# Performance work log

Hardware: AMD Instinct MI355X
Metric: run time of the kernel (lower is better)

The kernel has to match this reference:

```python
import jax, jax.numpy as jnp
import numpy as np

C = 32
SHIFTS = (1, 2, 4)
KSIZE = 4  # trans_layer: kernel KSIZE+1, stride KSIZE, pad KSIZE//2
EPS_NORM = 1e-12
EPS_BN = 1e-5


def _make_diff_kernels(c):
    # 8 fixed 3x3 difference kernels, tiled per channel for depthwise conv.
    d1 = np.array([[[-1, 0, 0], [0, 1, 0], [0, 0, 0]],
                   [[0, -1, 0], [0, 1, 0], [0, 0, 0]],
                   [[0, 0, -1], [0, 1, 0], [0, 0, 0]],
                   [[0, 0, 0], [0, 1, -1], [0, 0, 0]]], dtype=np.float32)
    d1 = d1.reshape(4, 1, 3, 3)
    d2 = d1[:, :, ::-1, ::-1].copy()
    delta = np.concatenate([d1, d2], axis=0)          # [8,1,3,3]
    return jnp.asarray(np.tile(delta, (c, 1, 1, 1)))  # [8C,1,3,3]


DIFF_KERNELS = _make_diff_kernels(C)


def conv2d(x, w, stride=1, pad=0, dilation=1, groups=1):
    return jax.lax.conv_general_dilated(
        x, w, (stride, stride), [(pad, pad), (pad, pad)],
        rhs_dilation=(dilation, dilation),
        dimension_numbers=('NCHW', 'OIHW', 'NCHW'),
        feature_group_count=groups)


def l2norm(x, axis=-1):
    n = jnp.sqrt(jnp.sum(x * x, axis=axis, keepdims=True))
    return x / jnp.maximum(n, EPS_NORM)


def setup_inputs() -> dict:
    key = jax.random.key(0)
    ks = jax.random.split(key, 8)
    S = len(SHIFTS)
    return {
        'cen': jax.random.normal(ks[0], (2, C, 256, 256), jnp.float32),
        'trans_W': jax.random.normal(ks[1], (C, C, 5, 5), jnp.float32) * 0.05,
        'trans_b': jax.random.normal(ks[2], (C,), jnp.float32) * 0.05,
        'query_W': jax.random.normal(ks[3], (C, C, 1, 1), jnp.float32) * 0.05,
        'value_W': jax.random.normal(ks[4], (S, C, C, 1, 1), jnp.float32) * 0.05,
        'key_W': jax.random.normal(ks[5], (S, C, C, 1, 1), jnp.float32) * 0.05,
        'out_W': jax.random.normal(ks[6], (C, C, 1, 1), jnp.float32) * 0.05,
        'bn_gamma': jnp.ones((C,), jnp.float32),
        'bn_beta': jnp.zeros((C,), jnp.float32),
        'bn_mean': jnp.zeros((C,), jnp.float32),
        'bn_var': jnp.ones((C,), jnp.float32),
    }


def reference(cen, trans_W, trans_b, query_W, value_W, key_W, out_W,
              bn_gamma, bn_beta, bn_mean, bn_var):
    b, _, w, h = cen.shape
    S = len(SHIFTS)
    size = (w * h) // (KSIZE * KSIZE)

    # trans_layer: kernel KSIZE+1, stride KSIZE, pad KSIZE//2
    kv_cen = conv2d(cen, trans_W, stride=KSIZE, pad=KSIZE // 2) \
        + trans_b[None, :, None, None]

    keys, values = [], []
    for i, d in enumerate(SHIFTS):
        v = conv2d(cen, value_W[i])          # [b,C,w,h]
        k = conv2d(kv_cen, key_W[i])         # [b,C,w',h']
        # depthwise dilated difference conv -> 8 outputs per channel
        v = conv2d(v, DIFF_KERNELS, pad=d, dilation=d, groups=C)  # [b,8C,w,h]
        k = conv2d(k, DIFF_KERNELS, pad=d, dilation=d, groups=C)  # [b,8C,w',h']
        keys.append(k)
        values.append(v)

    querys = conv2d(kv_cen, query_W)  # [b,C,w',h']

    keys = jnp.stack(keys, axis=2).reshape(b, C, 8 * S, size)       # [b,C,8S,size]
    values = jnp.stack(values, axis=2).reshape(b, C, 8 * S, w * h)  # [b,C,8S,wh]

    keys = jnp.swapaxes(l2norm(keys, -1), -2, -1)        # [b,C,size,8S]
    querys = l2norm(querys.reshape(b, C, 1, size), -1)   # [b,C,1,size]

    score = jnp.matmul(querys, keys)   # [b,C,1,8S]  cosine sims
    score = l2norm(score, -1)
    out = jnp.matmul(score, values).reshape(b, C, w, h)

    # out_conv: 1x1 conv -> BN (eval mode, running stats) -> ReLU
    out = conv2d(out, out_W)
    inv = jax.lax.rsqrt(bn_var + EPS_BN)
    out = (out - bn_mean[None, :, None, None]) * (bn_gamma * inv)[None, :, None, None] \
        + bn_beta[None, :, None, None]
    return jax.nn.relu(out)
```

## Files before the change

### kernel.cpp

```cpp
#include <hip/hip_runtime.h>
#include <hip/hip_bf16.h>


#define CC 32
#define HW 256
#define KVW 64

__global__ __launch_bounds__(256, 2) void k1_trans(const float* __restrict__ cen,
                                                   const float* __restrict__ tW,
                                                   const float* __restrict__ tB,
                                                   float* __restrict__ kv) {
  __shared__ alignas(16) float part[4][4][64];
  int bid = blockIdx.x;
  int b = bid >> 9, cog = (bid >> 6) & 7, y = bid & 63;
  int tid = threadIdx.x;
  int x = tid & 63;
  int w = __builtin_amdgcn_readfirstlane(tid >> 6);
  int ci0 = w * 8;
  int co0 = cog * 4;

  float acc[4] = {0.f, 0.f, 0.f, 0.f};
  const float4 z4 = {0.f, 0.f, 0.f, 0.f};

  int roff[5];
  bool rok[5];
#pragma unroll
  for (int r = 0; r < 5; r++) {
    int row = 4 * y - 2 + r;
    rok[r] = (row >= 0);
    roff[r] = (row < 0 ? 0 : row) * HW;
  }

  for (int cc4 = 0; cc4 < 8; cc4 += 4) {
    int ci = ci0 + cc4;
    const float* pc[4];
#pragma unroll
    for (int c = 0; c < 4; c++) pc[c] = cen + (size_t)(b * CC + ci + c) * 65536 + 4 * x;
    float4 A[4][5], B[4][5];
#pragma unroll
    for (int c = 0; c < 4; c++) {
#pragma unroll
      for (int r = 0; r < 5; r++) {
        A[c][r] = (x > 0) ? *(const float4*)(pc[c] + roff[r] - 4) : z4;
        B[c][r] = *(const float4*)(pc[c] + roff[r]);
      }
    }
#pragma unroll
    for (int r = 0; r < 5; r++) {
      if (!rok[r]) continue;
#pragma unroll
      for (int c = 0; c < 4; c++) {
#pragma unroll
        for (int co = 0; co < 4; co++) {
          const float* wa = tW + ((co0 + co) * CC + ci + c) * 25 + r * 5;
          acc[co] += wa[0] * A[c][r].z + wa[1] * A[c][r].w + wa[2] * B[c][r].x +
                     wa[3] * B[c][r].y + wa[4] * B[c][r].z;
        }
      }
    }
  }

#pragma unroll
  for (int co = 0; co < 4; co++) part[w][co][x] = acc[co];
  __syncthreads();

  {
    int co = tid >> 6, xx = tid & 63;
    float s = part[0][co][xx] + part[1][co][xx] + part[2][co][xx] + part[3][co][xx];
    kv[((b * CC + co0 + co) * KVW + y) * KVW + xx] = s + tB[co0 + co];
  }
}

__device__ inline float wred64(float v) {
#pragma unroll
  for (int off = 1; off < 64; off <<= 1) v += __shfl_xor(v, off);
  return v;
}

__global__ __launch_bounds__(1024) void k2i_partial(const float* __restrict__ kv,
                                                    const float* __restrict__ qW,
                                                    const float* __restrict__ kW,
                                                    float* __restrict__ pars) {
  __shared__ alignas(16) float kl[4096];
  __shared__ float wredl[16][18];
  int bid = blockIdx.x;
  int bc = bid / 3, i = bid - bc * 3;
  int b = bc >> 5, c = bc & 31;
  int tid = threadIdx.x;
  int lane = tid & 63, w = tid >> 6;
  int xx = tid & 63;
  int ybase = tid >> 6;

  float qreg[4];
#pragma unroll
  for (int r = 0; r < 4; r++) {
    int px = r * 1024 + tid;
    float q = 0.f, kk = 0.f;
    for (int ci = 0; ci < CC; ci++) {
      float val = kv[(b * CC + ci) * 4096 + px];
      q += qW[c * CC + ci] * val;
      kk += kW[(i * CC + c) * CC + ci] * val;
    }
    qreg[r] = q;
    kl[px] = kk;
  }
  __syncthreads();

  float q2 = 0.f;
#pragma unroll
  for (int r = 0; r < 4; r++) q2 += qreg[r] * qreg[r];
  q2 = wred64(q2);
  if (lane == 0) wredl[w][16] = q2;

  constexpr int DYt[8] = {-1, -1, -1, 0, 1, 1, 1, 0};
  constexpr int DXt[8] = {-1, 0, 1, 1, 1, 0, -1, -1};
  const int d = 1 << i;
#pragma unroll
  for (int n = 0; n < 8; n++) {
    const int dy = DYt[n], dx = DXt[n];
    int xn = xx + dx * d;
    bool xok = (xn >= 0 && xn < KVW);
    float dacc = 0.f, macc = 0.f;
#pragma unroll
    for (int r = 0; r < 4; r++) {
      int yy = r * 16 + ybase;
      int px = yy * KVW + xx;
      float kc = kl[px];
      int yn = yy + dy * d;
      float kn = (xok && yn >= 0 && yn < KVW) ? kl[yn * KVW + xn] : 0.f;
      float df = kc - kn;
      dacc += qreg[r] * df;
      macc += df * df;
    }
    dacc = wred64(dacc);
    macc = wred64(macc);
    if (lane == 0) {
      wredl[w][n] = dacc;
      wredl[w][8 + n] = macc;
    }
  }
  __syncthreads();

  float* pp = pars + (size_t)bid * 32;
  if (tid < 8) {
    float D = 0.f, M = 0.f;
    for (int w2 = 0; w2 < 16; w2++) {
      D += wredl[w2][tid];
      M += wredl[w2][8 + tid];
    }
    pp[tid] = D;
    pp[8 + tid] = M;
  }
  if (tid == 0) {
    float Q = 0.f;
    for (int w2 = 0; w2 < 16; w2++) Q += wredl[w2][16];
    pp[16] = Q;
  }
}

__global__ __launch_bounds__(64) void k2f_finalize(const float* __restrict__ pars,
                                                   float* __restrict__ scores) {
  __shared__ float srl[24];
  int bc = blockIdx.x;
  int t = threadIdx.x;
  if (t < 24) {
    int i = t >> 3, n = t & 7;
    const float* pp = pars + (size_t)(bc * 3 + i) * 32;
    float D = pp[n];
    float M = pp[8 + n];
    float Q = pars[(size_t)(bc * 3) * 32 + 16];
    float sr = D / (fmaxf(sqrtf(M), 1e-12f) * fmaxf(sqrtf(Q), 1e-12f));
    srl[t] = sr;
  }
  __syncthreads();
  if (t < 24) {
    float r2 = 0.f;
    for (int j = 0; j < 24; j++) r2 += srl[j] * srl[j];
    scores[bc * 24 + t] = srl[t] / fmaxf(sqrtf(r2), 1e-12f);
  }
}

__global__ __launch_bounds__(256) void k3a_values(const float* __restrict__ cen,
                                                  const float* __restrict__ vW,
                                                  __hip_bfloat16* __restrict__ v) {
  int bid = blockIdx.x;
  int b = bid >> 9, blk = bid & 511;
  int tid = threadIdx.x;
  int lane = tid & 63;
  int cg = __builtin_amdgcn_readfirstlane(tid >> 6);
  int px = blk * 128 + lane * 2;

  float2 cr[CC];
#pragma unroll
  for (int ci = 0; ci < CC; ci++)
    cr[ci] = *(const float2*)(cen + (size_t)(b * CC + ci) * 65536 + px);

#pragma unroll
  for (int i = 0; i < 3; i++) {
#pragma unroll
    for (int cc = 0; cc < 8; cc++) {
      int c = cg * 8 + cc;
      const float* wp = vW + (i * CC + c) * CC;
      float a0 = 0.f, a1 = 0.f;
#pragma unroll
      for (int ci = 0; ci < CC; ci++) {
        a0 += wp[ci] * cr[ci].x;
        a1 += wp[ci] * cr[ci].y;
      }
      __hip_bfloat16 h0 = __float2bfloat16(a0);
      __hip_bfloat16 h1 = __float2bfloat16(a1);
      unsigned int pk = (unsigned int)(*(unsigned short*)&h0) |
                        ((unsigned int)(*(unsigned short*)&h1) << 16);
      *(unsigned int*)((unsigned short*)v + (((size_t)((i * 2 + b) * CC + c)) << 16) +
                       px) = pk;
    }
  }
}

__global__ __launch_bounds__(256) void k3b_combine(const __hip_bfloat16* __restrict__ v,
                                                   const float* __restrict__ scores,
                                                   const float* __restrict__ oW,
                                                   const float* __restrict__ gamma,
                                                   const float* __restrict__ beta,
                                                   const float* __restrict__ mean,
                                                   const float* __restrict__ var,
                                                   float* __restrict__ out) {
  __shared__ alignas(16) float vt[3 * 24 * 24 * 4];
  __shared__ alignas(16) float sl[27][32];
  __shared__ alignas(16) float owl[32][32];
  __shared__ float bns[32], bnb[32];

  int bid = blockIdx.x;
  int b = bid >> 8, tile = bid & 255;
  int ty = tile >> 4, tx = tile & 15;
  int tid = threadIdx.x;
  int ly = tid >> 4, lx = tid & 15;

  for (int f = tid; f < 24 * 32; f += 256) {
    int j = f >> 5, c = f & 31;
    sl[j][c] = scores[(b * CC + c) * 24 + j];
  }
  for (int f = tid; f < 1024; f += 256) owl[f >> 5][f & 31] = oW[f];
  if (tid < 32) {
    float inv = rsqrtf(var[tid] + 1e-5f);
    float sc = gamma[tid] * inv;
    bns[tid] = sc;
    bnb[tid] = beta[tid] - mean[tid] * sc;
  }
  __syncthreads();
  if (tid < 32) {
#pragma unroll
    for (int i = 0; i < 3; i++) {
      float s = 0.f;
      for (int n = 0; n < 8; n++) s += sl[i * 8 + n][tid];
      sl[24 + i][tid] = s;
    }
  }

  int ldsoff[4], pxoff[4], ibase[4];
  bool okp[4];
#pragma unroll
  for (int it = 0; it < 4; it++) {
    int p = tid + it * 256;
    bool act = (p < 864);
    int pp = act ? p : 0;
    int i = pp / 288;
    int rem = pp - i * 288;
    int r = rem / 12;
    int col = (rem - r * 12) * 2;
    int gy = ty * 16 + r - 4, gx = tx * 16 + col - 4;
    okp[it] = act && gy >= 0 && gy < HW && gx >= 0 && gx < HW;
    pxoff[it] = gy * HW + gx;
    ibase[it] = (i * 2 + b) * CC;
    ldsoff[it] = ((i * 24 + r) * 24 + col) * 4;
  }

  constexpr int DYt[8] = {-1, -1, -1, 0, 1, 1, 1, 0};
  constexpr int DXt[8] = {-1, 0, 1, 1, 1, 0, -1, -1};

  float acc[32];
#pragma unroll
  for (int co = 0; co < 32; co++) acc[co] = 0.f;

  unsigned int pf[4][4];
  const unsigned short* vs = (const unsigned short*)v;

#pragma unroll
  for (int it = 0; it < 4; it++)
#pragma unroll
    for (int cp = 0; cp < 4; cp++)
      pf[it][cp] = okp[it]
                       ? *(const unsigned int*)(vs + (((size_t)(ibase[it] + cp)) << 16) +
                                                pxoff[it])
                       : 0u;

  for (int cg = 0; cg < 8; cg++) {
    __syncthreads();
#pragma unroll
    for (int it = 0; it < 4; it++) {
      if (it == 3 && tid >= 96) continue;
      float4 lo, hi;
      lo.x = __uint_as_float(pf[it][0] << 16);
      lo.y = __uint_as_float(pf[it][1] << 16);
      lo.z = __uint_as_float(pf[it][2] << 16);
      lo.w = __uint_as_float(pf[it][3] << 16);
      hi.x = __uint_as_float(pf[it][0] & 0xffff0000u);
      hi.y = __uint_as_float(pf[it][1] & 0xffff0000u);
      hi.z = __uint_as_float(pf[it][2] & 0xffff0000u);
      hi.w = __uint_as_float(pf[it][3] & 0xffff0000u);
      *(float4*)&vt[ldsoff[it]] = lo;
      *(float4*)&vt[ldsoff[it] + 4] = hi;
    }
    if (cg < 7) {
      int cb = (cg + 1) * 4;
#pragma unroll
      for (int it = 0; it < 4; it++)
#pragma unroll
        for (int cp = 0; cp < 4; cp++)
          pf[it][cp] = okp[it] ? *(const unsigned int*)(vs +
                                                        (((size_t)(ibase[it] + cb + cp))
                                                         << 16) +
                                                        pxoff[it])
                               : 0u;
    }
    __syncthreads();

    float4 pre = {0.f, 0.f, 0.f, 0.f};
#pragma unroll
    for (int i = 0; i < 3; i++) {
      const int d = 1 << i;
      float4 S4 = *(const float4*)&sl[24 + i][cg * 4];
      float4 ctr = *(const float4*)&vt[((i * 24 + (ly + 4)) * 24 + (lx + 4)) * 4];
      pre.x += S4.x * ctr.x;
      pre.y += S4.y * ctr.y;
      pre.z += S4.z * ctr.z;
      pre.w += S4.w * ctr.w;
#pragma unroll
      for (int n = 0; n < 8; n++) {
        float4 sj = *(const float4*)&sl[i * 8 + n][cg * 4];
        float4 nb = *(const float4*)&vt[((i * 24 + (ly + 4 + DYt[n] * d)) * 24 +
                                         (lx + 4 + DXt[n] * d)) * 4];
        pre.x -= sj.x * nb.x;
        pre.y -= sj.y * nb.y;
        pre.z -= sj.z * nb.z;
        pre.w -= sj.w * nb.w;
      }
    }
#pragma unroll
    for (int co = 0; co < 32; co++) {
      float4 ow = *(const float4*)&owl[co][cg * 4];
      acc[co] += ow.x * pre.x + ow.y * pre.y + ow.z * pre.z + ow.w * pre.w;
    }
  }

  int gy = ty * 16 + ly, gx = tx * 16 + lx;
#pragma unroll
  for (int co = 0; co < 32; co++) {
    float val = acc[co] * bns[co] + bnb[co];
    out[((size_t)(b * CC + co) << 16) + gy * HW + gx] = fmaxf(val, 0.f);
  }
}

extern "C" void kernel_launch(void* const* d_in, const int* in_sizes, int n_in,
                              void* d_out, int out_size, void* d_ws, size_t ws_size,
                              hipStream_t stream) {
  const float* cen = (const float*)d_in[0];
  const float* trans_W = (const float*)d_in[1];
  const float* trans_b = (const float*)d_in[2];
  const float* query_W = (const float*)d_in[3];
  const float* value_W = (const float*)d_in[4];
  const float* key_W = (const float*)d_in[5];
  const float* out_W = (const float*)d_in[6];
  const float* bn_gamma = (const float*)d_in[7];
  const float* bn_beta = (const float*)d_in[8];
  const float* bn_mean = (const float*)d_in[9];
  const float* bn_var = (const float*)d_in[10];
  float* out = (float*)d_out;

  float* kv = (float*)d_ws;
  float* scores = (float*)((char*)d_ws + 524288);
  __hip_bfloat16* v = (__hip_bfloat16*)((char*)d_ws + 532480);
  float* pars = (float*)((char*)d_ws + 25673728);

  k1_trans<<<1024, 256, 0, stream>>>(cen, trans_W, trans_b, kv);
  k2i_partial<<<192, 1024, 0, stream>>>(kv, query_W, key_W, pars);
  k2f_finalize<<<64, 64, 0, stream>>>(pars, scores);
  k3a_values<<<1024, 256, 0, stream>>>(cen, value_W, v);
  k3b_combine<<<512, 256, 0, stream>>>(v, scores, out_W, bn_gamma, bn_beta, bn_mean,
                                       bn_var, out);
}
```

Before: 169.7 us.

## Merge score-partial and value-projection kernels into one heterogeneous launch

Fuses the key/query score kernel and the value projection kernel into a single 448-block launch. The first 192 blocks compute scores and the remaining blocks compute bf16 values, so the two independent stages can run concurrently. The finalize kernel is removed: each score block computes its raw cosine score directly, and the final l2 normalisation over 24 entries moves into the combine kernel's prologue. The kv intermediate now lives in the output buffer, which is safe only because the last kernel overwrites it. The catch is that the fused kernel's 1024-thread launch bounds apply to the value path too, which may constrain its registers for the 32-element float2 array.

```diff
diff --git a/kernel.cpp b/kernel.cpp
--- a/kernel.cpp
+++ b/kernel.cpp
@@ -77,148 +77,123 @@
   return v;
 }
 
-__global__ __launch_bounds__(1024) void k2i_partial(const float* __restrict__ kv,
-                                                    const float* __restrict__ qW,
-                                                    const float* __restrict__ kW,
-                                                    float* __restrict__ pars) {
+__global__ __launch_bounds__(1024) void k23_fat(const float* __restrict__ kv,
+                                                const float* __restrict__ qW,
+                                                const float* __restrict__ kW,
+                                                float* __restrict__ srraw,
+                                                const float* __restrict__ cen,
+                                                const float* __restrict__ vW,
+                                                __hip_bfloat16* __restrict__ v) {
   __shared__ alignas(16) float kl[4096];
   __shared__ float wredl[16][18];
   int bid = blockIdx.x;
-  int bc = bid / 3, i = bid - bc * 3;
-  int b = bc >> 5, c = bc & 31;
   int tid = threadIdx.x;
-  int lane = tid & 63, w = tid >> 6;
-  int xx = tid & 63;
-  int ybase = tid >> 6;
-
-  float qreg[4];
-#pragma unroll
-  for (int r = 0; r < 4; r++) {
-    int px = r * 1024 + tid;
-    float q = 0.f, kk = 0.f;
-    for (int ci = 0; ci < CC; ci++) {
-      float val = kv[(b * CC + ci) * 4096 + px];
-      q += qW[c * CC + ci] * val;
-      kk += kW[(i * CC + c) * CC + ci] * val;
-    }
-    qreg[r] = q;
-    kl[px] = kk;
-  }
-  __syncthreads();
-
-  float q2 = 0.f;
-#pragma unroll
-  for (int r = 0; r < 4; r++) q2 += qreg[r] * qreg[r];
-  q2 = wred64(q2);
-  if (lane == 0) wredl[w][16] = q2;
-
-  constexpr int DYt[8] = {-1, -1, -1, 0, 1, 1, 1, 0};
-  constexpr int DXt[8] = {-1, 0, 1, 1, 1, 0, -1, -1};
-  const int d = 1 << i;
-#pragma unroll
-  for (int n = 0; n < 8; n++) {
-    const int dy = DYt[n], dx = DXt[n];
-    int xn = xx + dx * d;
-    bool xok = (xn >= 0 && xn < KVW);
-    float dacc = 0.f, macc = 0.f;
+
+  if (bid < 192) {
+    int bc = bid / 3, i = bid - bc * 3;
+    int b = bc >> 5, c = bc & 31;
+    int lane = tid & 63, w = tid >> 6;
+    int xx = tid & 63;
+    int ybase = tid >> 6;
+
+    float qreg[4];
 #pragma unroll
     for (int r = 0; r < 4; r++) {
-      int yy = r * 16 + ybase;
-      int px = yy * KVW + xx;
-      float kc = kl[px];
-      int yn = yy + dy * d;
-      float kn = (xok && yn >= 0 && yn < KVW) ? kl[yn * KVW + xn] : 0.f;
-      float df = kc - kn;
-      dacc += qreg[r] * df;
-      macc += df * df;
-    }
-    dacc = wred64(dacc);
-    macc = wred64(macc);
-    if (lane == 0) {
-      wredl[w][n] = dacc;
-      wredl[w][8 + n] = macc;
-    }
-  }
-  __syncthreads();
-
-  float* pp = pars + (size_t)bid * 32;
-  if (tid < 8) {
-    float D = 0.f, M = 0.f;
-    for (int w2 = 0; w2 < 16; w2++) {
-      D += wredl[w2][tid];
-      M += wredl[w2][8 + tid];
-    }
-    pp[tid] = D;
-    pp[8 + tid] = M;
-  }
-  if (tid == 0) {
-    float Q = 0.f;
-    for (int w2 = 0; w2 < 16; w2++) Q += wredl[w2][16];
-    pp[16] = Q;
-  }
-}
-
-__global__ __launch_bounds__(64) void k2f_finalize(const float* __restrict__ pars,
-                                                   float* __restrict__ scores) {
-  __shared__ float srl[24];
-  int bc = blockIdx.x;
-  int t = threadIdx.x;
-  if (t < 24) {
-    int i = t >> 3, n = t & 7;
-    const float* pp = pars + (size_t)(bc * 3 + i) * 32;
-    float D = pp[n];
-    float M = pp[8 + n];
-    float Q = pars[(size_t)(bc * 3) * 32 + 16];
-    float sr = D / (fmaxf(sqrtf(M), 1e-12f) * fmaxf(sqrtf(Q), 1e-12f));
-    srl[t] = sr;
-  }
-  __syncthreads();
-  if (t < 24) {
-    float r2 = 0.f;
-    for (int j = 0; j < 24; j++) r2 += srl[j] * srl[j];
-    scores[bc * 24 + t] = srl[t] / fmaxf(sqrtf(r2), 1e-12f);
-  }
-}
-
-__global__ __launch_bounds__(256) void k3a_values(const float* __restrict__ cen,
-                                                  const float* __restrict__ vW,
-                                                  __hip_bfloat16* __restrict__ v) {
-  int bid = blockIdx.x;
-  int b = bid >> 9, blk = bid & 511;
-  int tid = threadIdx.x;
-  int lane = tid & 63;
-  int cg = __builtin_amdgcn_readfirstlane(tid >> 6);
-  int px = blk * 128 + lane * 2;
-
-  float2 cr[CC];
-#pragma unroll
-  for (int ci = 0; ci < CC; ci++)
-    cr[ci] = *(const float2*)(cen + (size_t)(b * CC + ci) * 65536 + px);
-
-#pragma unroll
-  for (int i = 0; i < 3; i++) {
-#pragma unroll
-    for (int cc = 0; cc < 8; cc++) {
-      int c = cg * 8 + cc;
-      const float* wp = vW + (i * CC + c) * CC;
-      float a0 = 0.f, a1 = 0.f;
-#pragma unroll
+      int px = r * 1024 + tid;
+      float q = 0.f, kk = 0.f;
       for (int ci = 0; ci < CC; ci++) {
-        a0 += wp[ci] * cr[ci].x;
-        a1 += wp[ci] * cr[ci].y;
-      }
-      __hip_bfloat16 h0 = __float2bfloat16(a0);
-      __hip_bfloat16 h1 = __float2bfloat16(a1);
-      unsigned int pk = (unsigned int)(*(unsigned short*)&h0) |
-                        ((unsigned int)(*(unsigned short*)&h1) << 16);
-      *(unsigned int*)((unsigned short*)v + (((size_t)((i * 2 + b) * CC + c)) << 16) +
-                       px) = pk;
+        float val = kv[(b * CC + ci) * 4096 + px];
+        q += qW[c * CC + ci] * val;
+        kk += kW[(i * CC + c) * CC + ci] * val;
+      }
+      qreg[r] = q;
+      kl[px] = kk;
+    }
+    __syncthreads();
+
+    float q2 = 0.f;
+#pragma unroll
+    for (int r = 0; r < 4; r++) q2 += qreg[r] * qreg[r];
+    q2 = wred64(q2);
+    if (lane == 0) wredl[w][16] = q2;
+
+    constexpr int DYt[8] = {-1, -1, -1, 0, 1, 1, 1, 0};
+    constexpr int DXt[8] = {-1, 0, 1, 1, 1, 0, -1, -1};
+    const int d = 1 << i;
+#pragma unroll
+    for (int n = 0; n < 8; n++) {
+      const int dy = DYt[n], dx = DXt[n];
+      int xn = xx + dx * d;
+      bool xok = (xn >= 0 && xn < KVW);
+      float dacc = 0.f, macc = 0.f;
+#pragma unroll
+      for (int r = 0; r < 4; r++) {
+        int yy = r * 16 + ybase;
+        int px = yy * KVW + xx;
+        float kc = kl[px];
+        int yn = yy + dy * d;
+        float kn = (xok && yn >= 0 && yn < KVW) ? kl[yn * KVW + xn] : 0.f;
+        float df = kc - kn;
+        dacc += qreg[r] * df;
+        macc += df * df;
+      }
+      dacc = wred64(dacc);
+      macc = wred64(macc);
+      if (lane == 0) {
+        wredl[w][n] = dacc;
+        wredl[w][8 + n] = macc;
+      }
+    }
+    __syncthreads();
+
+    if (tid < 8) {
+      float D = 0.f, M = 0.f, Q = 0.f;
+      for (int w2 = 0; w2 < 16; w2++) {
+        D += wredl[w2][tid];
+        M += wredl[w2][8 + tid];
+        Q += wredl[w2][16];
+      }
+      float sr = D / (fmaxf(sqrtf(M), 1e-12f) * fmaxf(sqrtf(Q), 1e-12f));
+      srraw[bc * 24 + i * 8 + tid] = sr;
+    }
+  } else {
+    int bid2 = bid - 192;
+    int vb = bid2 * 4 + (tid >> 8);
+    int b = vb >> 9, blk = vb & 511;
+    int lane = tid & 63;
+    int cg = __builtin_amdgcn_readfirstlane((tid >> 6) & 3);
+    int px = blk * 128 + lane * 2;
+
+    float2 cr[CC];
+#pragma unroll
+    for (int ci = 0; ci < CC; ci++)
+      cr[ci] = *(const float2*)(cen + (size_t)(b * CC + ci) * 65536 + px);
+
+#pragma unroll
+    for (int i = 0; i < 3; i++) {
+#pragma unroll
+      for (int cc = 0; cc < 8; cc++) {
+        int c = cg * 8 + cc;
+        const float* wp = vW + (i * CC + c) * CC;
+        float a0 = 0.f, a1 = 0.f;
+#pragma unroll
+        for (int ci = 0; ci < CC; ci++) {
+          a0 += wp[ci] * cr[ci].x;
+          a1 += wp[ci] * cr[ci].y;
+        }
+        __hip_bfloat16 h0 = __float2bfloat16(a0);
+        __hip_bfloat16 h1 = __float2bfloat16(a1);
+        unsigned int pk = (unsigned int)(*(unsigned short*)&h0) |
+                          ((unsigned int)(*(unsigned short*)&h1) << 16);
+        *(unsigned int*)((unsigned short*)v + (((size_t)((i * 2 + b) * CC + c)) << 16) +
+                         px) = pk;
+      }
     }
   }
 }
 
 __global__ __launch_bounds__(256) void k3b_combine(const __hip_bfloat16* __restrict__ v,
-                                                   const float* __restrict__ scores,
+                                                   const float* __restrict__ srraw,
                                                    const float* __restrict__ oW,
                                                    const float* __restrict__ gamma,
                                                    const float* __restrict__ beta,
@@ -236,9 +211,9 @@
   int tid = threadIdx.x;
   int ly = tid >> 4, lx = tid & 15;
 
-  for (int f = tid; f < 24 * 32; f += 256) {
+  for (int f = tid; f < 768; f += 256) {
     int j = f >> 5, c = f & 31;
-    sl[j][c] = scores[(b * CC + c) * 24 + j];
+    sl[j][c] = srraw[(b * CC + c) * 24 + j];
   }
   for (int f = tid; f < 1024; f += 256) owl[f >> 5][f & 31] = oW[f];
   if (tid < 32) {
@@ -249,6 +224,15 @@
   }
   __syncthreads();
   if (tid < 32) {
+    float r2 = 0.f;
+#pragma unroll
+    for (int j = 0; j < 24; j++) {
+      float s = sl[j][tid];
+      r2 += s * s;
+    }
+    float dn = fmaxf(sqrtf(r2), 1e-12f);
+#pragma unroll
+    for (int j = 0; j < 24; j++) sl[j][tid] /= dn;
 #pragma unroll
     for (int i = 0; i < 3; i++) {
       float s = 0.f;
@@ -377,15 +361,12 @@
   const float* bn_var = (const float*)d_in[10];
   float* out = (float*)d_out;
 
-  float* kv = (float*)d_ws;
-  float* scores = (float*)((char*)d_ws + 524288);
+  float* kv = (float*)d_out;
+  float* srraw = (float*)d_ws;
   __hip_bfloat16* v = (__hip_bfloat16*)((char*)d_ws + 532480);
-  float* pars = (float*)((char*)d_ws + 25673728);
 
   k1_trans<<<1024, 256, 0, stream>>>(cen, trans_W, trans_b, kv);
-  k2i_partial<<<192, 1024, 0, stream>>>(kv, query_W, key_W, pars);
-  k2f_finalize<<<64, 64, 0, stream>>>(pars, scores);
-  k3a_values<<<1024, 256, 0, stream>>>(cen, value_W, v);
-  k3b_combine<<<512, 256, 0, stream>>>(v, scores, out_W, bn_gamma, bn_beta, bn_mean,
+  k23_fat<<<448, 1024, 0, stream>>>(kv, query_W, key_W, srraw, cen, value_W, v);
+  k3b_combine<<<512, 256, 0, stream>>>(v, srraw, out_W, bn_gamma, bn_beta, bn_mean,
                                        bn_var, out);
 }
```

New measurement: 164.8 us. 1.03x faster.
